# Optimization experiments

Hardware: AMD Instinct MI355X
Metric: run time of the kernel (lower is better)

## Reference

```python
import jax, jax.numpy as jnp
import numpy as np

B, S, D, E = 8, 4096, 1024, 3
EPS = 1e-5


def setup_inputs() -> dict:
    key = jax.random.key(0)
    ks = jax.random.split(key, 4)
    s = 0.02  # init scale for weights
    return {
        "inputs": jax.random.normal(ks[0], (B, S, D), jnp.float32),
        "current_state": jnp.zeros((B, D), jnp.float32),
        "norm_w": jnp.ones((D,), jnp.float32),              # RMSNorm weight
        "router_w": jax.random.normal(ks[1], (D, E), jnp.float32) * s,
        "router_b": jnp.zeros((E,), jnp.float32),
        "w_gh": jax.random.normal(ks[2], (E, D, 2 * D), jnp.float32) * s,  # per-expert minGRU hidden+gate proj
        "w_out": jax.random.normal(ks[3], (E, D, D), jnp.float32) * s,     # per-expert proj_out
    }


def _rmsnorm(x, w, eps=EPS):
    return x * jax.lax.rsqrt(jnp.mean(x * x, axis=-1, keepdims=True) + eps) * w


def _g(x):
    # minGRU continuous activation g(x) = x + 0.5 for x >= 0 else sigmoid(x)
    return jnp.where(x >= 0, x + 0.5, jax.nn.sigmoid(x))


def reference(inputs, current_state, norm_w, router_w, router_b, w_gh, w_out):
    x = _rmsnorm(inputs, norm_w)                       # [B,S,D]
    # SMEAR: route per sample (mean-pooled features), soft-merge expert weights
    logits = jnp.mean(x, axis=1) @ router_w + router_b  # [B,E]
    probs = jax.nn.softmax(logits, axis=-1)             # [B,E]
    Wg = jnp.einsum('be,eij->bij', probs, w_gh)         # [B,D,2D] merged gate/hidden weights
    Wo = jnp.einsum('be,eij->bij', probs, w_out)        # [B,D,D]  merged output proj
    hg = jnp.einsum('bsi,bij->bsj', x, Wg)              # [B,S,2D]
    hid, gate = jnp.split(hg, 2, axis=-1)
    z = jax.nn.sigmoid(gate)                            # update gate
    a = 1.0 - z                                         # decay coefficient
    b = z * _g(hid)                                     # input term
    # fold initial state into first step: h_0 contribution
    b = b.at[:, 0].add(a[:, 0] * current_state)
    # linear recurrence h_t = a_t * h_{t-1} + b_t via associative scan over time
    def comb(c1, c2):
        a1, b1 = c1
        a2, b2 = c2
        return a1 * a2, a2 * b1 + b2
    _, h = jax.lax.associative_scan(comb, (a, b), axis=1)  # [B,S,D]
    new_state = h[:, -1]
    out = jnp.einsum('bsi,bij->bsj', h, Wo) + inputs       # proj_out + residual
    aux_loss = jnp.float32(0.0)
    return out, new_state, aux_loss
```

## Files before the change

### kernel.cpp

```cpp
#include <hip/hip_runtime.h>
#include <hip/hip_bf16.h>
#include <cstdint>
#include <cstddef>

using bf16 = __bf16;
typedef __bf16 bf16x8 __attribute__((ext_vector_type(8)));
typedef __bf16 bf16x4 __attribute__((ext_vector_type(4)));
typedef float  f32x4  __attribute__((ext_vector_type(4)));

#define DEV __device__ __forceinline__

DEV float sigmoidf_(float x) { return 1.0f / (1.0f + __expf(-x)); }

typedef __attribute__((address_space(1))) void as1_void;
typedef __attribute__((address_space(3))) void as3_void;

DEV void load16_lds(const void* g, void* l) {
  __builtin_amdgcn_global_load_lds((as1_void*)(void*)g, (as3_void*)l, 16, 0, 0);
}

__global__ __launch_bounds__(256) void k_rms_colsum(const float* __restrict__ inp,
                                                    const float* __restrict__ nw,
                                                    bf16* __restrict__ x,
                                                    float* __restrict__ part) {
  const int b = blockIdx.y, c = blockIdx.x;
  const int w = threadIdx.x >> 6, lane = threadIdx.x & 63;
  __shared__ float sC[4][1024];
  f32x4 wv[4];
  #pragma unroll
  for (int k = 0; k < 4; ++k) wv[k] = *(const f32x4*)(nw + lane * 16 + k * 4);
  f32x4 accp[4] = {};
  const size_t rowbase = (size_t)b * 4096 + (size_t)c * 64;
  #pragma unroll 4
  for (int i = 0; i < 16; ++i) {
    const int row = w * 16 + i;
    const float* r = inp + (rowbase + row) * 1024 + lane * 16;
    f32x4 v[4];
    #pragma unroll
    for (int k = 0; k < 4; ++k) v[k] = *(const f32x4*)(r + k * 4);
    float ss = 0.f;
    #pragma unroll
    for (int k = 0; k < 4; ++k)
      ss += v[k][0]*v[k][0] + v[k][1]*v[k][1] + v[k][2]*v[k][2] + v[k][3]*v[k][3];
    #pragma unroll
    for (int off = 32; off; off >>= 1) ss += __shfl_xor(ss, off);
    const float sc = rsqrtf(ss * (1.0f / 1024.0f) + 1e-5f);
    bf16* xo = x + (rowbase + row) * 1024 + lane * 16;
    #pragma unroll
    for (int k = 0; k < 4; ++k) {
      f32x4 nv;
      nv[0] = v[k][0] * sc * wv[k][0]; nv[1] = v[k][1] * sc * wv[k][1];
      nv[2] = v[k][2] * sc * wv[k][2]; nv[3] = v[k][3] * sc * wv[k][3];
      accp[k][0] += nv[0]; accp[k][1] += nv[1];
      accp[k][2] += nv[2]; accp[k][3] += nv[3];
      bf16x4 o;
      o[0] = (bf16)nv[0]; o[1] = (bf16)nv[1]; o[2] = (bf16)nv[2]; o[3] = (bf16)nv[3];
      *(bf16x4*)(xo + k * 4) = o;
    }
  }
  #pragma unroll
  for (int k = 0; k < 4; ++k) *(f32x4*)(&sC[w][lane * 16 + k * 4]) = accp[k];
  __syncthreads();
  const int t = threadIdx.x;
  f32x4 s = *(const f32x4*)(&sC[0][t * 4]);
  s += *(const f32x4*)(&sC[1][t * 4]);
  s += *(const f32x4*)(&sC[2][t * 4]);
  s += *(const f32x4*)(&sC[3][t * 4]);
  *(f32x4*)(part + ((size_t)(b * 64 + c)) * 1024 + t * 4) = s;
}

__global__ __launch_bounds__(256) void k_router(const float* __restrict__ part,
                                                const float* __restrict__ rw,
                                                const float* __restrict__ rb,
                                                float* __restrict__ probs,
                                                float* __restrict__ aux) {
  const int b = blockIdx.x;
  const int t = threadIdx.x;
  __shared__ float red[4];
  __shared__ float lg[3];
  f32x4 cs = {0.f, 0.f, 0.f, 0.f};
  #pragma unroll 8
  for (int c = 0; c < 64; ++c)
    cs += *(const f32x4*)(part + ((size_t)(b * 64 + c)) * 1024 + t * 4);
  for (int e = 0; e < 3; ++e) {
    float dot = cs[0] * rw[(t*4+0)*3+e] + cs[1] * rw[(t*4+1)*3+e]
              + cs[2] * rw[(t*4+2)*3+e] + cs[3] * rw[(t*4+3)*3+e];
    for (int off = 32; off; off >>= 1) dot += __shfl_down(dot, off);
    if ((t & 63) == 0) red[t >> 6] = dot;
    __syncthreads();
    if (t == 0) lg[e] = (red[0]+red[1]+red[2]+red[3]) * (1.0f/4096.0f) + rb[e];
    __syncthreads();
  }
  if (t == 0) {
    float m = fmaxf(lg[0], fmaxf(lg[1], lg[2]));
    float p0 = __expf(lg[0]-m), p1 = __expf(lg[1]-m), p2 = __expf(lg[2]-m);
    float inv = 1.0f / (p0 + p1 + p2);
    probs[b*3+0] = p0*inv; probs[b*3+1] = p1*inv; probs[b*3+2] = p2*inv;
    if (b == 0) *aux = 0.0f;
  }
}

__global__ __launch_bounds__(256) void k_mixT2(const float* __restrict__ Wg,
                                               const float* __restrict__ Wo,
                                               const float* __restrict__ probs,
                                               bf16* __restrict__ og,
                                               bf16* __restrict__ oo) {
  const int xb = blockIdx.x;
  const float* W; bf16* out; int Ncols; int j0;
  if (xb < 32) { W = Wg; out = og; Ncols = 2048; j0 = xb * 64; }
  else         { W = Wo; out = oo; Ncols = 1024; j0 = (xb - 32) * 64; }
  const int b = blockIdx.z;
  const int i0 = blockIdx.y * 64;
  const float p0 = probs[b*3+0], p1 = probs[b*3+1], p2 = probs[b*3+2];
  __shared__ float tile[64][68];
  const int t = threadIdx.x;
  const int jl = (t & 15) * 4;
  const size_t estr = (size_t)1024 * Ncols;
  for (int ii = 0; ii < 4; ++ii) {
    int il = (t >> 4) + ii * 16;
    const float* src = W + (size_t)(i0 + il) * Ncols + (j0 + jl);
    f32x4 v0 = *(const f32x4*)(src);
    f32x4 v1 = *(const f32x4*)(src + estr);
    f32x4 v2 = *(const f32x4*)(src + 2 * estr);
    f32x4 v = p0 * v0 + p1 * v1 + p2 * v2;
    tile[il][jl+0] = v[0]; tile[il][jl+1] = v[1];
    tile[il][jl+2] = v[2]; tile[il][jl+3] = v[3];
  }
  __syncthreads();
  bf16* ob = out + (size_t)b * Ncols * 1024;
  const int il2 = (t & 15) * 4;
  for (int jj = 0; jj < 4; ++jj) {
    int jl2 = (t >> 4) + jj * 16;
    bf16x4 o;
    o[0] = (bf16)tile[il2+0][jl2]; o[1] = (bf16)tile[il2+1][jl2];
    o[2] = (bf16)tile[il2+2][jl2]; o[3] = (bf16)tile[il2+3][jl2];
    *(bf16x4*)(ob + (size_t)(j0 + jl2) * 1024 + (i0 + il2)) = o;
  }
}

template<int EPI>
__global__ __launch_bounds__(512, 1) void k_gemm256(const bf16* __restrict__ A,
                                                    const bf16* __restrict__ Bt,
                                                    const float* __restrict__ addend,
                                                    float* __restrict__ Cout,
                                                    bf16* __restrict__ pa,
                                                    bf16* __restrict__ pb,
                                                    int M, int N, int K) {
  const int bz = blockIdx.z;
  const int nx = gridDim.x;
  const int nwg = nx * gridDim.y;
  const int orig = blockIdx.y * nx + blockIdx.x;
  const int swz = (orig & 7) * (nwg >> 3) + (orig >> 3);
  const int tm = swz / nx, tn = swz % nx;

  __shared__ __align__(16) char smem[131072];
  const int tid = threadIdx.x;
  const int lane = tid & 63, w = tid >> 6;
  const int l15 = lane & 15, quad = lane >> 4;
  const int wm = (w >> 2) * 128;
  const int wn = (w & 3) * 64;

  const bf16* Ab  = A  + (size_t)bz * M * K;
  const bf16* Btb = Bt + (size_t)bz * N * K;

  const int row0 = tid >> 3,          kc0 = (tid & 7) ^ (row0 & 7);
  const int row1 = (512 + tid) >> 3,  kc1 = (tid & 7) ^ (row1 & 7);

  auto browf = [&](int c) -> int {
    if constexpr (EPI == 0) {
      return tn * 128 + ((c >> 6) * 32) + (c & 31) + (((c & 63) >= 32) ? 1024 : 0);
    } else {
      return tn * 256 + c;
    }
  };
  const bf16* aS0_0 = Ab + (size_t)(tm*256 +       row0) * K + kc0 * 8;
  const bf16* aS0_1 = Ab + (size_t)(tm*256 +       row1) * K + kc1 * 8;
  const bf16* aS1_0 = Ab + (size_t)(tm*256 + 128 + row0) * K + kc0 * 8;
  const bf16* aS1_1 = Ab + (size_t)(tm*256 + 128 + row1) * K + kc1 * 8;
  const bf16* bS0_0 = Btb + (size_t)browf(row0)       * K + kc0 * 8;
  const bf16* bS0_1 = Btb + (size_t)browf(row1)       * K + kc1 * 8;
  const bf16* bS1_0 = Btb + (size_t)browf(128 + row0) * K + kc0 * 8;
  const bf16* bS1_1 = Btb + (size_t)browf(128 + row1) * K + kc1 * 8;

  const int ld0 = tid * 16;
  const int ld1 = 8192 + tid * 16;
  auto stage = [&](int buf, int u) {
    load16_lds(aS0_0 + u*64, smem + buf*32768 + ld0);
    load16_lds(aS0_1 + u*64, smem + buf*32768 + ld1);
    load16_lds(aS1_0 + u*64, smem + buf*32768 + 16384 + ld0);
    load16_lds(aS1_1 + u*64, smem + buf*32768 + 16384 + ld1);
    load16_lds(bS0_0 + u*64, smem + 65536 + buf*32768 + ld0);
    load16_lds(bS0_1 + u*64, smem + 65536 + buf*32768 + ld1);
    load16_lds(bS1_0 + u*64, smem + 65536 + buf*32768 + 16384 + ld0);
    load16_lds(bS1_1 + u*64, smem + 65536 + buf*32768 + 16384 + ld1);
  };

  f32x4 acc[8][4] = {};
  bf16x8 a[4][2], b0[2][2], b1[2][2];

  auto ldA = [&](int buf, int mq) {
    const bf16* base = (const bf16*)(smem + buf*32768);
    #pragma unroll
    for (int mi = 0; mi < 4; ++mi) {
      const int m = wm + mq*64 + mi*16 + l15;
      #pragma unroll
      for (int ks = 0; ks < 2; ++ks) {
        const int kc = ks*4 + quad;
        a[mi][ks] = *(const bf16x8*)(base + (size_t)(m*8 + (kc ^ (m & 7))) * 8);
      }
    }
  };
  auto ldB = [&](int buf, int nq, bf16x8 (&bb)[2][2]) {
    const bf16* base = (const bf16*)(smem + 65536 + buf*32768);
    #pragma unroll
    for (int ni = 0; ni < 2; ++ni) {
      const int n = wn + nq*32 + ni*16 + l15;
      #pragma unroll
      for (int ks = 0; ks < 2; ++ks) {
        const int kc = ks*4 + quad;
        bb[ni][ks] = *(const bf16x8*)(base + (size_t)(n*8 + (kc ^ (n & 7))) * 8);
      }
    }
  };

#define MMAC(MQ, NQ, BB)                                                        \
  _Pragma("unroll")                                                             \
  for (int mi = 0; mi < 4; ++mi) {                                              \
    _Pragma("unroll")                                                           \
    for (int ni = 0; ni < 2; ++ni) {                                            \
      f32x4 c_ = acc[(MQ)*4 + mi][(NQ)*2 + ni];                                 \
      c_ = __builtin_amdgcn_mfma_f32_16x16x32_bf16(a[mi][0], BB[ni][0], c_, 0, 0, 0); \
      c_ = __builtin_amdgcn_mfma_f32_16x16x32_bf16(a[mi][1], BB[ni][1], c_, 0, 0, 0); \
      acc[(MQ)*4 + mi][(NQ)*2 + ni] = c_;                                       \
    }                                                                           \
  }

  const int NT = K >> 6;

  stage(0, 0);
  __syncthreads();

  for (int t = 0; t < NT; ++t) {
    const int buf = t & 1;
    if (t + 1 < NT) stage(buf ^ 1, t + 1);
    ldA(buf, 0);
    ldB(buf, 0, b0);
    MMAC(0, 0, b0);
    ldB(buf, 1, b1);
    MMAC(0, 1, b1);
    ldA(buf, 1);
    MMAC(1, 1, b1);
    MMAC(1, 0, b0);
    __syncthreads();
  }

  if constexpr (EPI == 0) {
    bf16* Aab = pa + (size_t)bz * M * 1024;
    bf16* Bab = pb + (size_t)bz * M * 1024;
    const int jb = tn * 128 + (w & 3) * 32;
    const int rb = tm * 256 + wm;
    #pragma unroll
    for (int mi = 0; mi < 8; ++mi)
      #pragma unroll
      for (int ni = 0; ni < 2; ++ni)
        #pragma unroll
        for (int r = 0; r < 4; ++r) {
          const int srow = rb + mi * 16 + quad * 4 + r;
          float hid = acc[mi][ni][r];
          float gt  = acc[mi][ni + 2][r];
          float z = sigmoidf_(gt);
          float av = 1.0f - z;
          float gv = (hid >= 0.0f) ? (hid + 0.5f) : sigmoidf_(hid);
          float bv = z * gv;
          size_t oidx = (size_t)srow * 1024 + jb + ni * 16 + l15;
          Aab[oidx] = (bf16)av;
          Bab[oidx] = (bf16)bv;
        }
  } else {
    float* sC = (float*)smem;
    const int ST = 260;
    float* C = Cout + (size_t)bz * M * N;
    const float* Ain = addend + (size_t)bz * M * N;
    #pragma unroll
    for (int p = 0; p < 8; ++p) {
      if ((w >> 2) == (p >> 2)) {
        const int mi0 = (p & 3) * 2;
        #pragma unroll
        for (int mm = 0; mm < 2; ++mm)
          #pragma unroll
          for (int nt_ = 0; nt_ < 4; ++nt_)
            #pragma unroll
            for (int r = 0; r < 4; ++r) {
              const int rl = mm * 16 + quad * 4 + r;
              sC[rl * ST + (w & 3) * 64 + nt_ * 16 + l15] = acc[mi0 + mm][nt_][r];
            }
      }
      __syncthreads();
      #pragma unroll
      for (int i = 0; i < 4; ++i) {
        const int v = i * 512 + tid;
        const int rl = v >> 6, c4 = (v & 63) * 4;
        const int grow = tm * 256 + p * 32 + rl;
        const int gcol = tn * 256 + c4;
        f32x4 cv = *(f32x4*)(sC + rl * ST + c4);
        f32x4 ad = *(const f32x4*)(Ain + (size_t)grow * N + gcol);
        *(f32x4*)(C + (size_t)grow * N + gcol) = cv + ad;
      }
      __syncthreads();
    }
  }
#undef MMAC
}

__global__ __launch_bounds__(256) void k_scan1(const bf16* __restrict__ Aab,
                                               const bf16* __restrict__ Bab,
                                               float* __restrict__ cA,
                                               float* __restrict__ cB) {
  const int b = blockIdx.y, c = blockIdx.x;
  const int d = threadIdx.x * 4;
  f32x4 A = {1.f, 1.f, 1.f, 1.f}, Bv = {0.f, 0.f, 0.f, 0.f};
  const size_t base = ((size_t)(b * 4096 + c * 64)) * 1024 + d;
  #pragma unroll 4
  for (int i = 0; i < 64; ++i) {
    bf16x4 av = *(const bf16x4*)(Aab + base + (size_t)i * 1024);
    bf16x4 bv = *(const bf16x4*)(Bab + base + (size_t)i * 1024);
    #pragma unroll
    for (int j = 0; j < 4; ++j) {
      float a = (float)av[j], bb = (float)bv[j];
      A[j] *= a; Bv[j] = a * Bv[j] + bb;
    }
  }
  *(f32x4*)(cA + ((size_t)(b * 64 + c)) * 1024 + d) = A;
  *(f32x4*)(cB + ((size_t)(b * 64 + c)) * 1024 + d) = Bv;
}

__global__ __launch_bounds__(256) void k_scan2(const float* __restrict__ cA,
                                               const float* __restrict__ cB,
                                               const float* __restrict__ state,
                                               float* __restrict__ hin,
                                               float* __restrict__ ns) {
  const int gid = blockIdx.x * 256 + threadIdx.x;
  const int b = gid >> 10, d = gid & 1023;
  float h = state[gid];
  for (int c0 = 0; c0 < 64; c0 += 8) {
    float ar[8], br[8];
    #pragma unroll
    for (int i = 0; i < 8; ++i) {
      size_t idx = (((size_t)(b * 64 + c0 + i)) << 10) + d;
      ar[i] = cA[idx]; br[i] = cB[idx];
    }
    #pragma unroll
    for (int i = 0; i < 8; ++i) {
      size_t idx = (((size_t)(b * 64 + c0 + i)) << 10) + d;
      hin[idx] = h;
      h = ar[i] * h + br[i];
    }
  }
  ns[gid] = h;
}

__global__ __launch_bounds__(256) void k_scan3(const bf16* __restrict__ Aab,
                                               const bf16* __restrict__ Bab,
                                               const float* __restrict__ hin,
                                               bf16* __restrict__ hq) {
  const int b = blockIdx.y, c = blockIdx.x;
  const int d = threadIdx.x * 4;
  f32x4 h = *(const f32x4*)(hin + ((size_t)(b * 64 + c)) * 1024 + d);
  const size_t base = ((size_t)(b * 4096 + c * 64)) * 1024 + d;
  bf16* ob = hq + base;
  #pragma unroll 4
  for (int i = 0; i < 64; ++i) {
    bf16x4 av = *(const bf16x4*)(Aab + base + (size_t)i * 1024);
    bf16x4 bv = *(const bf16x4*)(Bab + base + (size_t)i * 1024);
    bf16x4 o;
    #pragma unroll
    for (int j = 0; j < 4; ++j) {
      h[j] = (float)av[j] * h[j] + (float)bv[j];
      o[j] = (bf16)h[j];
    }
    *(bf16x4*)(ob + (size_t)i * 1024) = o;
  }
}

extern "C" void kernel_launch(void* const* d_in, const int* in_sizes, int n_in,
                              void* d_out, int out_size, void* d_ws, size_t ws_size,
                              hipStream_t stream) {
  const float* inputs   = (const float*)d_in[0];
  const float* state    = (const float*)d_in[1];
  const float* norm_w   = (const float*)d_in[2];
  const float* router_w = (const float*)d_in[3];
  const float* router_b = (const float*)d_in[4];
  const float* w_gh     = (const float*)d_in[5];
  const float* w_out    = (const float*)d_in[6];

  float* out = (float*)d_out;
  float* new_state = out + (size_t)8 * 4096 * 1024;
  float* aux = new_state + 8 * 1024;

  char* ws = (char*)d_ws;
  size_t off = 0;
  auto alloc = [&](size_t bytes) {
    char* p = ws + off;
    off = (off + bytes + 255) & ~(size_t)255;
    return p;
  };
  bf16*  x    = (bf16*)alloc((size_t)8 * 4096 * 1024 * 2);
  bf16*  a_ar = (bf16*)alloc((size_t)8 * 4096 * 1024 * 2);
  bf16*  b_ar = (bf16*)alloc((size_t)8 * 4096 * 1024 * 2);
  bf16*  hq   = (bf16*)alloc((size_t)8 * 4096 * 1024 * 2);
  bf16*  WgT  = (bf16*)alloc((size_t)8 * 2048 * 1024 * 2);
  bf16*  WoT  = (bf16*)alloc((size_t)8 * 1024 * 1024 * 2);
  float* part = (float*)alloc((size_t)8 * 64 * 1024 * 4);
  float* probs = (float*)alloc(256);
  float* cA   = (float*)alloc((size_t)8 * 64 * 1024 * 4);
  float* cB   = (float*)alloc((size_t)8 * 64 * 1024 * 4);
  float* hin  = (float*)alloc((size_t)8 * 64 * 1024 * 4);
  (void)in_sizes; (void)n_in; (void)out_size; (void)ws_size;

  k_rms_colsum<<<dim3(64, 8), 256, 0, stream>>>(inputs, norm_w, x, part);
  k_router <<<8, 256, 0, stream>>>(part, router_w, router_b, probs, aux);
  k_mixT2  <<<dim3(48, 16, 8), 256, 0, stream>>>(w_gh, w_out, probs, WgT, WoT);
  k_gemm256<0><<<dim3(8, 16, 8), 512, 0, stream>>>(x, WgT, nullptr, nullptr,
                                                   a_ar, b_ar, 4096, 2048, 1024);
  k_scan1 <<<dim3(64, 8), 256, 0, stream>>>(a_ar, b_ar, cA, cB);
  k_scan2 <<<32, 256, 0, stream>>>(cA, cB, state, hin, new_state);
  k_scan3 <<<dim3(64, 8), 256, 0, stream>>>(a_ar, b_ar, hin, hq);
  k_gemm256<1><<<dim3(4, 16, 8), 512, 0, stream>>>(hq, WoT, inputs, out,
                                                   nullptr, nullptr, 4096, 1024, 1024);
}
```

Measured before the change: 629.8 us.

## Fuse scan chunk-summary pass into gate GEMM epilogue and coalesce RMSNorm loads

The first GEMM epilogue now computes, per 64-row chunk, the composed decay and input terms of the linear recurrence. It does this from fp32 accumulator values using shared-memory partials, which removes the separate k_scan1 kernel that re-read the bf16 a/b arrays from global memory. This saves one kernel launch and a full read of both large intermediate arrays, at the cost of a longer epilogue with an extra barrier. The RMSNorm kernel's lane-to-column mapping is also changed so that consecutive lanes access consecutive 16-byte segments, giving coalesced loads and stores.

```diff
diff --git a/kernel.cpp b/kernel.cpp
--- a/kernel.cpp
+++ b/kernel.cpp
@@ -28,16 +28,16 @@
   __shared__ float sC[4][1024];
   f32x4 wv[4];
   #pragma unroll
-  for (int k = 0; k < 4; ++k) wv[k] = *(const f32x4*)(nw + lane * 16 + k * 4);
+  for (int k = 0; k < 4; ++k) wv[k] = *(const f32x4*)(nw + k * 256 + lane * 4);
   f32x4 accp[4] = {};
   const size_t rowbase = (size_t)b * 4096 + (size_t)c * 64;
   #pragma unroll 4
   for (int i = 0; i < 16; ++i) {
     const int row = w * 16 + i;
-    const float* r = inp + (rowbase + row) * 1024 + lane * 16;
+    const float* r = inp + (rowbase + row) * 1024 + lane * 4;
     f32x4 v[4];
     #pragma unroll
-    for (int k = 0; k < 4; ++k) v[k] = *(const f32x4*)(r + k * 4);
+    for (int k = 0; k < 4; ++k) v[k] = *(const f32x4*)(r + k * 256);
     float ss = 0.f;
     #pragma unroll
     for (int k = 0; k < 4; ++k)
@@ -45,7 +45,7 @@
     #pragma unroll
     for (int off = 32; off; off >>= 1) ss += __shfl_xor(ss, off);
     const float sc = rsqrtf(ss * (1.0f / 1024.0f) + 1e-5f);
-    bf16* xo = x + (rowbase + row) * 1024 + lane * 16;
+    bf16* xo = x + (rowbase + row) * 1024 + lane * 4;
     #pragma unroll
     for (int k = 0; k < 4; ++k) {
       f32x4 nv;
@@ -55,11 +55,11 @@
       accp[k][2] += nv[2]; accp[k][3] += nv[3];
       bf16x4 o;
       o[0] = (bf16)nv[0]; o[1] = (bf16)nv[1]; o[2] = (bf16)nv[2]; o[3] = (bf16)nv[3];
-      *(bf16x4*)(xo + k * 4) = o;
+      *(bf16x4*)(xo + k * 256) = o;
     }
   }
   #pragma unroll
-  for (int k = 0; k < 4; ++k) *(f32x4*)(&sC[w][lane * 16 + k * 4]) = accp[k];
+  for (int k = 0; k < 4; ++k) *(f32x4*)(&sC[w][k * 256 + lane * 4]) = accp[k];
   __syncthreads();
   const int t = threadIdx.x;
   f32x4 s = *(const f32x4*)(&sC[0][t * 4]);
@@ -145,6 +145,8 @@
                                                     float* __restrict__ Cout,
                                                     bf16* __restrict__ pa,
                                                     bf16* __restrict__ pb,
+                                                    float* __restrict__ cA,
+                                                    float* __restrict__ cB,
                                                     int M, int N, int K) {
   const int bz = blockIdx.z;
   const int nx = gridDim.x;
@@ -257,12 +259,15 @@
   if constexpr (EPI == 0) {
     bf16* Aab = pa + (size_t)bz * M * 1024;
     bf16* Bab = pb + (size_t)bz * M * 1024;
+    float* sRunA = (float*)smem;
+    float* sRunB = (float*)(smem + 32768);
     const int jb = tn * 128 + (w & 3) * 32;
     const int rb = tm * 256 + wm;
     #pragma unroll
     for (int mi = 0; mi < 8; ++mi)
       #pragma unroll
-      for (int ni = 0; ni < 2; ++ni)
+      for (int ni = 0; ni < 2; ++ni) {
+        float Ar = 1.f, Br = 0.f;
         #pragma unroll
         for (int r = 0; r < 4; ++r) {
           const int srow = rb + mi * 16 + quad * 4 + r;
@@ -275,7 +280,31 @@
           size_t oidx = (size_t)srow * 1024 + jb + ni * 16 + l15;
           Aab[oidx] = (bf16)av;
           Bab[oidx] = (bf16)bv;
+          Br = av * Br + bv;
+          Ar = av * Ar;
         }
+        const int chunkL = (wm >> 6) + (mi >> 2);
+        const int colL   = (w & 3) * 32 + ni * 16 + l15;
+        const int idx    = ((mi & 3) * 4 + quad) * 512 + chunkL * 128 + colL;
+        sRunA[idx] = Ar;
+        sRunB[idx] = Br;
+      }
+    __syncthreads();
+    {
+      const int chunk = tid >> 7, colL = tid & 127;
+      float Acc = 1.f, Bcc = 0.f;
+      #pragma unroll
+      for (int s = 0; s < 16; ++s) {
+        const float Ar = sRunA[s * 512 + chunk * 128 + colL];
+        const float Br = sRunB[s * 512 + chunk * 128 + colL];
+        Bcc = Ar * Bcc + Br;
+        Acc = Ar * Acc;
+      }
+      const int gchunk = tm * 4 + chunk;
+      const int gd = tn * 128 + colL;
+      cA[(((size_t)(bz * 64 + gchunk)) << 10) + gd] = Acc;
+      cB[(((size_t)(bz * 64 + gchunk)) << 10) + gd] = Bcc;
+    }
   } else {
     float* sC = (float*)smem;
     const int ST = 260;
@@ -310,28 +339,6 @@
     }
   }
 #undef MMAC
-}
-
-__global__ __launch_bounds__(256) void k_scan1(const bf16* __restrict__ Aab,
-                                               const bf16* __restrict__ Bab,
-                                               float* __restrict__ cA,
-                                               float* __restrict__ cB) {
-  const int b = blockIdx.y, c = blockIdx.x;
-  const int d = threadIdx.x * 4;
-  f32x4 A = {1.f, 1.f, 1.f, 1.f}, Bv = {0.f, 0.f, 0.f, 0.f};
-  const size_t base = ((size_t)(b * 4096 + c * 64)) * 1024 + d;
-  #pragma unroll 4
-  for (int i = 0; i < 64; ++i) {
-    bf16x4 av = *(const bf16x4*)(Aab + base + (size_t)i * 1024);
-    bf16x4 bv = *(const bf16x4*)(Bab + base + (size_t)i * 1024);
-    #pragma unroll
-    for (int j = 0; j < 4; ++j) {
-      float a = (float)av[j], bb = (float)bv[j];
-      A[j] *= a; Bv[j] = a * Bv[j] + bb;
-    }
-  }
-  *(f32x4*)(cA + ((size_t)(b * 64 + c)) * 1024 + d) = A;
-  *(f32x4*)(cB + ((size_t)(b * 64 + c)) * 1024 + d) = Bv;
 }
 
 __global__ __launch_bounds__(256) void k_scan2(const float* __restrict__ cA,
@@ -421,10 +428,11 @@
   k_router <<<8, 256, 0, stream>>>(part, router_w, router_b, probs, aux);
   k_mixT2  <<<dim3(48, 16, 8), 256, 0, stream>>>(w_gh, w_out, probs, WgT, WoT);
   k_gemm256<0><<<dim3(8, 16, 8), 512, 0, stream>>>(x, WgT, nullptr, nullptr,
-                                                   a_ar, b_ar, 4096, 2048, 1024);
-  k_scan1 <<<dim3(64, 8), 256, 0, stream>>>(a_ar, b_ar, cA, cB);
+                                                   a_ar, b_ar, cA, cB,
+                                                   4096, 2048, 1024);
   k_scan2 <<<32, 256, 0, stream>>>(cA, cB, state, hin, new_state);
   k_scan3 <<<dim3(64, 8), 256, 0, stream>>>(a_ar, b_ar, hin, hq);
   k_gemm256<1><<<dim3(4, 16, 8), 512, 0, stream>>>(hq, WoT, inputs, out,
-                                                   nullptr, nullptr, 4096, 1024, 1024);
-}
+                                                   nullptr, nullptr, nullptr, nullptr,
+                                                   4096, 1024, 1024);
+}
```

Measured after the change: 615.3 us. 2.3% less time.
